# Kernel tuning notes

Hardware: AMD Instinct MI355X
Metric: run time of the kernel (lower is better)

Reference implementation:

```python
import jax, jax.numpy as jnp
import numpy as np

B, S, D, M, O = 16, 1024, 1024, 1024, 1024


def _sq_cdist(x1, x2):
    # squared euclidean distance, shapes (..., n, d) x (..., m, d) -> (..., n, m)
    n1 = jnp.sum(x1 * x1, axis=-1, keepdims=True)            # (..., n, 1)
    n2 = jnp.sum(x2 * x2, axis=-1)[..., None, :]             # (..., 1, m)
    cross = jnp.einsum('...nd,...md->...nm', x1, x2)
    return jnp.maximum(n1 + n2 - 2.0 * cross, 0.0)


def _rbf(x1, x2, log_lengthscale):
    ls2 = jnp.exp(log_lengthscale) ** 2
    return jnp.exp(-0.5 * _sq_cdist(x1, x2) / ls2)


def setup_inputs() -> dict:
    key = jax.random.key(0)
    k1, k2, k3 = jax.random.split(key, 3)
    x = jax.random.normal(k1, (B, S, D), dtype=jnp.float32)
    inducing_points = jax.random.normal(k2, (M, D), dtype=jnp.float32)
    log_lengthscale = jnp.zeros((1,), dtype=jnp.float32)
    log_noise = jnp.zeros((1,), dtype=jnp.float32)
    # nn.Linear(n_inducing, output_dim).weight has shape (O, M)
    lim = 1.0 / np.sqrt(M)
    W_out = jax.random.uniform(k3, (O, M), minval=-lim, maxval=lim, dtype=jnp.float32)
    return {
        'x': x,
        'inducing_points': inducing_points,
        'log_lengthscale': log_lengthscale,
        'log_noise': log_noise,
        'W_out': W_out,
        'num_sentences': S,
    }


def reference(x, inducing_points, log_lengthscale, log_noise, W_out, num_sentences):
    ll = log_lengthscale[0]
    K_xx = _rbf(x, x, ll)                                    # (B, S, S)
    K_xi = _rbf(x, inducing_points[None], ll)                # (B, S, M)
    K_ii = _rbf(inducing_points, inducing_points, ll)        # (M, M)
    K_ii_reg = K_ii + jnp.exp(log_noise[0]) * jnp.eye(M, dtype=x.dtype)
    K_ii_inv = jnp.linalg.inv(K_ii_reg)                      # (M, M)
    A = jnp.einsum('bsm,mk->bsk', K_xi, K_ii_inv)            # (B, S, M)
    mean = jnp.einsum('bsm,om->bso', A, W_out)               # (B, S, O)
    var = K_xx - jnp.einsum('bsm,btm->bst', A, K_xi)         # (B, S, S)
    var_diag = jnp.diagonal(var, axis1=-2, axis2=-1)         # (B, S)
    var_out = jnp.broadcast_to(var_diag[..., None], (x.shape[0], num_sentences, W_out.shape[0]))
    return mean, jax.nn.softplus(var_out)
```

## Files before the change

### kernel.cpp

```cpp
#include <hip/hip_runtime.h>
#include <hip/hip_bf16.h>
#include <math.h>


typedef unsigned short u16;
typedef __attribute__((ext_vector_type(8))) short short8;
typedef __attribute__((ext_vector_type(4))) float f32x4;
typedef __attribute__((ext_vector_type(4))) unsigned short us4;

__device__ __forceinline__ float bf2f(u16 b) {
  union { unsigned u; float f; } x; x.u = ((unsigned)b) << 16; return x.f;
}
__device__ __forceinline__ u16 f2bf(float f) {
  union { float f; unsigned u; } x; x.f = f;
  unsigned r = x.u + 0x7fffu + ((x.u >> 16) & 1u);
  return (u16)(r >> 16);
}

__device__ __forceinline__ void gl_lds16(const void* g, void* l) {
  __builtin_amdgcn_global_load_lds(
      (const __attribute__((address_space(1))) void*)g,
      (__attribute__((address_space(3))) void*)l, 16, 0, 0);
}

__device__ __forceinline__ float local_cmax(const float* rs, float* sm) {
  float m = 0.f;
  for (int i = threadIdx.x; i < 1024; i += 256) m = fmaxf(m, rs[i]);
#pragma unroll
  for (int o = 32; o > 0; o >>= 1) m = fmaxf(m, __shfl_xor(m, o));
  __syncthreads();
  if ((threadIdx.x & 63) == 0) sm[threadIdx.x >> 6] = m;
  __syncthreads();
  return 1.0f / fmaxf(fmaxf(sm[0], sm[1]), fmaxf(sm[2], sm[3]));
}

template <int EPI>
__device__ __forceinline__ void big_body(
    int bid, u16* lds,
    const u16* Ag, const u16* Bg,
    float* outF, float* varF, u16* outB,
    const float* rowN, const float* colN,
    const float* p_ll, float* qb) {
  constexpr int NT = 16;
  const int tid = threadIdx.x;
  const int lane = tid & 63;
  const int wave = tid >> 6;
  const int wr = wave >> 1, wc = wave & 1;
  const int fro = lane & 15, khi = lane >> 4;
  size_t brow, bcol;
  if (EPI == 3) {
    brow = (size_t)(bid >> 3);
    bcol = (size_t)(bid & 7);
  } else {
    const int xcd = bid & 7, j7 = bid >> 3;
    brow = (size_t)(xcd * 16 + (j7 >> 3));
    bcol = (size_t)(j7 & 7);
  }

  if (EPI == 0) {
    if (tid < 16) qb[(size_t)bid * 16 + tid] = 0.0f;
  }

  f32x4 acc[4][4] = {};

  auto stageA = [&](int tt, int bb) {
#pragma unroll
    for (int c = 0; c < 4; ++c) {
      const int ci = tid + 256 * c;
      const int row = ci >> 3;
      const int gk = (ci & 7) ^ (row & 7);
      gl_lds16(Ag + (size_t)(brow * 128 + row) * 1024 + tt * 64 + gk * 8,
               &lds[bb * 16384 + ci * 8]);
    }
  };
  auto stageB = [&](int tt, int bb) {
#pragma unroll
    for (int c = 0; c < 4; ++c) {
      const int ci = tid + 256 * c;
      const int row = ci >> 3;
      const int gk = (ci & 7) ^ (row & 7);
      gl_lds16(Bg + (size_t)(bcol * 128 + row) * 1024 + tt * 64 + gk * 8,
               &lds[bb * 16384 + 8192 + ci * 8]);
    }
  };

  stageA(0, 0);
  stageB(0, 0);
  stageB(1, 1);
  asm volatile("s_waitcnt vmcnt(4)" ::: "memory");
  __builtin_amdgcn_s_barrier();

  for (int t = 0; t < NT; ++t) {
    const int cb = t & 1;
    const int ab = cb * 16384;
    const int bb = cb * 16384 + 8192;
    short8 bfrag[4][2];
#pragma unroll
    for (int p = 0; p < 4; ++p) {
      short8 afr[2];
      const int rr = wr * 64 + p * 16 + fro;
#pragma unroll
      for (int s = 0; s < 2; ++s) {
        const int kl = (s * 4 + khi) ^ (rr & 7);
        afr[s] = *(const short8*)&lds[ab + (rr * 8 + kl) * 8];
      }
      if (p == 0) {
#pragma unroll
        for (int n = 0; n < 4; ++n) {
          const int cc = wc * 64 + n * 16 + fro;
#pragma unroll
          for (int s = 0; s < 2; ++s) {
            const int kl = (s * 4 + khi) ^ (cc & 7);
            bfrag[n][s] = *(const short8*)&lds[bb + (cc * 8 + kl) * 8];
          }
        }
        if (t + 1 < NT) stageA(t + 1, cb ^ 1);
      } else if (p == 1) {
        if (t + 2 < NT) stageB(t + 2, cb);
      }
      __builtin_amdgcn_s_setprio(1);
#pragma unroll
      for (int n = 0; n < 4; ++n)
#pragma unroll
        for (int s = 0; s < 2; ++s)
          acc[p][n] = __builtin_amdgcn_mfma_f32_16x16x32_bf16(
              afr[s], bfrag[n][s], acc[p][n], 0, 0, 0);
      __builtin_amdgcn_s_setprio(0);
      if (p == 3) {
        if (t < NT - 2) asm volatile("s_waitcnt vmcnt(4)" ::: "memory");
        else            asm volatile("s_waitcnt vmcnt(0)" ::: "memory");
      }
      __builtin_amdgcn_s_barrier();
    }
  }

  float inv2 = 0.f, cc2 = 0.f, ss2 = 0.f;
  if (EPI == 0) inv2 = 0.5f * expf(-2.0f * p_ll[0]);
  if (EPI == 3) {
    __syncthreads();
    cc2 = local_cmax(rowN, (float*)lds);
    ss2 = sqrtf(cc2);
  }
#pragma unroll
  for (int m = 0; m < 4; m++) {
#pragma unroll
    for (int j = 0; j < 4; j++) {
      const size_t grow = brow * 128 + wr * 64 + m * 16 + khi * 4 + j;
      float rn = 0.f, sp = 0.f;
      if (EPI == 0) rn = rowN[grow];
      if (EPI == 1) {
        float vq = 1.0f - qb[grow];
        sp = fmaxf(vq, 0.f) + log1pf(expf(-fabsf(vq)));
      }
      float part = 0.f;
#pragma unroll
      for (int n = 0; n < 4; n++) {
        const size_t gcol = bcol * 128 + wc * 64 + n * 16 + fro;
        const size_t o = grow * 1024 + gcol;
        float v = acc[m][n][j];
        if (EPI == 0) {
          float d2 = fmaxf(rn + colN[gcol] - 2.0f * v, 0.0f);
          outB[o] = f2bf(expf(-inv2 * d2));
        } else if (EPI == 1) {
          outF[o] = v;
          varF[o] = sp;
        } else if (EPI == 3) {
          float idv = (grow == gcol) ? 1.0f : 0.0f;
          outB[o] = f2bf(ss2 * (1.5f * idv - 0.5f * cc2 * bf2f(Ag[o]) +
                                0.6875f * bf2f(Bg[o]) - 0.3125f * cc2 * v));
        } else {
          part += v * v;
        }
      }
      if (EPI == 2) {
        part += __shfl_xor(part, 1);
        part += __shfl_xor(part, 2);
        part += __shfl_xor(part, 4);
        part += __shfl_xor(part, 8);
        if (fro == 0) atomicAdd(&qb[grow], part);
      }
    }
  }
}

__device__ __forceinline__ void small_core(const u16* Ap, const u16* Bp,
                                           u16* As, u16* Bs,
                                           f32x4 (&acc)[4][4]) {
  const int tid = threadIdx.x;
  const int lane = tid & 63;
  const int wave = tid >> 6;
  const int wr = wave >> 1, wc = wave & 1;
  const int idx0 = tid, idx1 = tid + 256;
  const u16* gA0 = Ap + (size_t)(idx0 >> 2) * 1024 + (size_t)(idx0 & 3) * 8;
  const u16* gA1 = Ap + (size_t)(idx1 >> 2) * 1024 + (size_t)(idx1 & 3) * 8;
  const u16* gB0 = Bp + (size_t)(idx0 >> 2) * 1024 + (size_t)(idx0 & 3) * 8;
  const u16* gB1 = Bp + (size_t)(idx1 >> 2) * 1024 + (size_t)(idx1 & 3) * 8;
  u16* lA0 = &As[idx0 * 8]; u16* lA1 = &As[idx1 * 8];
  u16* lB0 = &Bs[idx0 * 8]; u16* lB1 = &Bs[idx1 * 8];
  const int fro = lane & 15;
  const int ko = (lane >> 4) * 8;

  for (int kt = 0; kt < 1024; kt += 32) {
    gl_lds16(gA0 + kt, lA0);
    gl_lds16(gA1 + kt, lA1);
    gl_lds16(gB0 + kt, lB0);
    gl_lds16(gB1 + kt, lB1);
    __syncthreads();
    short8 af[4], bfr[4];
#pragma unroll
    for (int m = 0; m < 4; m++) {
      af[m]  = *(const short8*)&As[(wr * 64 + m * 16 + fro) * 32 + ko];
      bfr[m] = *(const short8*)&Bs[(wc * 64 + m * 16 + fro) * 32 + ko];
    }
#pragma unroll
    for (int m = 0; m < 4; m++)
#pragma unroll
      for (int n = 0; n < 4; n++)
        acc[m][n] = __builtin_amdgcn_mfma_f32_16x16x32_bf16(af[m], bfr[n], acc[m][n], 0, 0, 0);
    __syncthreads();
  }
}

__device__ __forceinline__ void kii_body(int bid, u16* lds,
                                         const u16* ipb, u16* kii,
                                         const float* ni, const float* ll,
                                         const float* ln, float* rs) {
  const int by = bid >> 3, bx = bid & 7;
  f32x4 acc[4][4] = {};
  small_core(ipb + (size_t)by * 131072, ipb + (size_t)bx * 131072,
             lds, lds + 4096, acc);
  const int lane = threadIdx.x & 63;
  const int wave = threadIdx.x >> 6;
  const int wr = wave >> 1, wc = wave & 1;
  float inv2 = 0.5f * expf(-2.0f * ll[0]);
  float noise = expf(ln[0]);
#pragma unroll
  for (int m = 0; m < 4; m++)
#pragma unroll
    for (int j = 0; j < 4; j++) {
      const size_t grow = by * 128 + wr * 64 + m * 16 + (lane >> 4) * 4 + j;
      float rn = ni[grow];
      float part = 0.f;
#pragma unroll
      for (int n = 0; n < 4; n++) {
        const size_t gcol = bx * 128 + wc * 64 + n * 16 + (lane & 15);
        float d2 = fmaxf(rn + ni[gcol] - 2.0f * acc[m][n][j], 0.0f);
        float kv = (grow == gcol) ? (1.0f + noise) : expf(-inv2 * d2);
        kii[grow * 1024 + gcol] = f2bf(kv);
        part += fabsf(kv);
      }
      part += __shfl_xor(part, 1);
      part += __shfl_xor(part, 2);
      part += __shfl_xor(part, 4);
      part += __shfl_xor(part, 8);
      if ((lane & 15) == 0) atomicAdd(&rs[grow], part);
    }
}

__device__ __forceinline__ void batch1_body(int bid, u16* lds,
                                            const u16* kii, const u16* Wb,
                                            u16* R2b, u16* T1b,
                                            const float* rs) {
  const int z = bid >> 6, r = bid & 63;
  const int by = r >> 3, bx = r & 7;
  f32x4 acc[4][4] = {};
  const u16* Abase = z ? Wb : kii;
  small_core(Abase + (size_t)by * 131072, kii + (size_t)bx * 131072,
             lds, lds + 4096, acc);
  __syncthreads();
  const float c = local_cmax(rs, (float*)lds);
  const int lane = threadIdx.x & 63;
  const int wave = threadIdx.x >> 6;
  const int wr = wave >> 1, wc = wave & 1;
#pragma unroll
  for (int m = 0; m < 4; m++)
#pragma unroll
    for (int j = 0; j < 4; j++) {
      const size_t grow = by * 128 + wr * 64 + m * 16 + (lane >> 4) * 4 + j;
#pragma unroll
      for (int n = 0; n < 4; n++) {
        const size_t gcol = bx * 128 + wc * 64 + n * 16 + (lane & 15);
        const size_t o = grow * 1024 + gcol;
        float v = acc[m][n][j];
        if (z == 0) {
          float idv = (grow == gcol) ? 1.0f : 0.0f;
          R2b[o] = f2bf(idv - 2.0f * c * bf2f(kii[o]) + c * c * v);
        } else {
          T1b[o] = f2bf(2.0f * bf2f(Wb[o]) - c * v);
        }
      }
    }
}

__device__ __forceinline__ void batch2b_body(int by, int bx, u16* lds,
                                             const u16* R2b, const u16* T1b,
                                             u16* U, const float* rs) {
  f32x4 acc[4][4] = {};
  small_core(T1b + (size_t)by * 131072, R2b + (size_t)bx * 131072,
             lds, lds + 4096, acc);
  __syncthreads();
  const float c = local_cmax(rs, (float*)lds);
  const int lane = threadIdx.x & 63;
  const int wave = threadIdx.x >> 6;
  const int wr = wave >> 1, wc = wave & 1;
#pragma unroll
  for (int m = 0; m < 4; m++)
#pragma unroll
    for (int j = 0; j < 4; j++) {
      const size_t grow = by * 128 + wr * 64 + m * 16 + (lane >> 4) * 4 + j;
#pragma unroll
      for (int n = 0; n < 4; n++) {
        const size_t gcol = bx * 128 + wc * 64 + n * 16 + (lane & 15);
        const size_t o = grow * 1024 + gcol;
        U[o + 1048576] = f2bf(c * (bf2f(T1b[o]) + acc[m][n][j]));
      }
    }
}

__device__ __forceinline__ void prepx_body(int bid, u16* lds,
                                           const float* x, u16* xbf,
                                           float* nx) {
  float* wsum = (float*)lds;
  for (int r = bid; r < 16384; r += 2048) {
    const float4 v = ((const float4*)(x + (size_t)r * 1024))[threadIdx.x];
    float ss = v.x * v.x + v.y * v.y + v.z * v.z + v.w * v.w;
    us4 o; o.x = f2bf(v.x); o.y = f2bf(v.y); o.z = f2bf(v.z); o.w = f2bf(v.w);
    ((us4*)(xbf + (size_t)r * 1024))[threadIdx.x] = o;
#pragma unroll
    for (int s = 32; s > 0; s >>= 1) ss += __shfl_xor(ss, s);
    if ((threadIdx.x & 63) == 0) wsum[threadIdx.x >> 6] = ss;
    __syncthreads();
    if (threadIdx.x == 0) nx[r] = wsum[0] + wsum[1] + wsum[2] + wsum[3];
    __syncthreads();
  }
}

__global__ __launch_bounds__(256) void fat1(
    const float* __restrict__ x, u16* __restrict__ xbf, float* __restrict__ nx,
    const u16* __restrict__ ipb, u16* __restrict__ kii,
    const float* __restrict__ ni, const float* __restrict__ ll,
    const float* __restrict__ ln, float* __restrict__ rs) {
  __shared__ u16 lds[8192];
  const int bid = blockIdx.x;
  if (bid < 64) kii_body(bid, lds, ipb, kii, ni, ll, ln, rs);
  else          prepx_body(bid - 64, lds, x, xbf, nx);
}

__global__ __launch_bounds__(256, 2) void fat2(
    const u16* __restrict__ xbf, const u16* __restrict__ ipb,
    u16* __restrict__ kxib,
    const float* __restrict__ nx, const float* __restrict__ ni,
    const float* __restrict__ ll, float* __restrict__ qb,
    const u16* __restrict__ kii, const u16* __restrict__ wbf,
    u16* __restrict__ R2b, u16* __restrict__ t1b,
    const float* __restrict__ rs) {
  __shared__ u16 lds[32768];
  const int bid = blockIdx.x;
  if (bid < 128) batch1_body(bid, lds, kii, wbf, R2b, t1b, rs);
  else big_body<0>(bid - 128, lds, xbf, ipb, nullptr, nullptr, kxib,
                   nx, ni, ll, qb);
}

__global__ __launch_bounds__(256, 2) void gemm_s(
    const u16* __restrict__ kii, const u16* __restrict__ R2b,
    u16* __restrict__ U, const float* __restrict__ rs) {
  __shared__ u16 lds[32768];
  big_body<3>(blockIdx.x, lds, kii, R2b, nullptr, nullptr, U,
              rs, nullptr, nullptr, nullptr);
}

__global__ __launch_bounds__(256, 2) void fat3(
    const u16* __restrict__ kxib, const u16* __restrict__ U,
    float* __restrict__ qb,
    const u16* __restrict__ R2b, const u16* __restrict__ t1b,
    u16* __restrict__ Uw, const float* __restrict__ rs) {
  __shared__ u16 lds[32768];
  const int bid = blockIdx.x;
  if (bid < 64) batch2b_body(bid >> 3, bid & 7, lds, R2b, t1b, Uw, rs);
  else big_body<2>(bid - 64, lds, kxib, U, nullptr, nullptr, nullptr,
                   nullptr, nullptr, nullptr, qb);
}

__global__ __launch_bounds__(256, 2) void kmean(
    const u16* __restrict__ kxib, const u16* __restrict__ w2t,
    float* __restrict__ meanO, float* __restrict__ varO,
    float* __restrict__ qb) {
  __shared__ u16 lds[32768];
  big_body<1>(blockIdx.x, lds, kxib, w2t, meanO, varO, nullptr,
              nullptr, nullptr, nullptr, qb);
}

__global__ __launch_bounds__(256) void prep_ipw(const float* __restrict__ ip,
                                                const float* __restrict__ W,
                                                u16* __restrict__ ipb,
                                                u16* __restrict__ wbf,
                                                float* __restrict__ ni,
                                                float* __restrict__ rs) {
  __shared__ float wsum[4];
  int b = blockIdx.x;
  if (b < 1024) {
    const float4 v = ((const float4*)(ip + (size_t)b * 1024))[threadIdx.x];
    float ss = v.x * v.x + v.y * v.y + v.z * v.z + v.w * v.w;
    us4 o; o.x = f2bf(v.x); o.y = f2bf(v.y); o.z = f2bf(v.z); o.w = f2bf(v.w);
    ((us4*)(ipb + (size_t)b * 1024))[threadIdx.x] = o;
#pragma unroll
    for (int s = 32; s > 0; s >>= 1) ss += __shfl_xor(ss, s);
    if ((threadIdx.x & 63) == 0) wsum[threadIdx.x >> 6] = ss;
    __syncthreads();
    if (threadIdx.x == 0) {
      ni[b] = wsum[0] + wsum[1] + wsum[2] + wsum[3];
      rs[b] = 0.0f;
    }
  } else {
    int r = b - 1024;
    const float4 v = ((const float4*)(W + (size_t)r * 1024))[threadIdx.x];
    us4 o; o.x = f2bf(v.x); o.y = f2bf(v.y); o.z = f2bf(v.z); o.w = f2bf(v.w);
    ((us4*)(wbf + (size_t)r * 1024))[threadIdx.x] = o;
  }
}

extern "C" void kernel_launch(void* const* d_in, const int* in_sizes, int n_in,
                              void* d_out, int out_size, void* d_ws, size_t ws_size,
                              hipStream_t stream) {
  const float* x  = (const float*)d_in[0];
  const float* ip = (const float*)d_in[1];
  const float* ll = (const float*)d_in[2];
  const float* ln = (const float*)d_in[3];
  const float* W  = (const float*)d_in[4];

  char* ws = (char*)d_ws;
  const size_t MB = 1ull << 20;
  u16* kxib = (u16*)(ws + 0 * MB);
  u16* xbf  = (u16*)(ws + 32 * MB);
  u16* ipb  = (u16*)(ws + 64 * MB);
  u16* wbf  = (u16*)(ws + 66 * MB);
  u16* kii  = (u16*)(ws + 68 * MB);
  u16* R2b  = (u16*)(ws + 70 * MB);
  u16* Ub   = (u16*)(ws + 74 * MB);
  u16* t1b  = (u16*)(ws + 78 * MB);
  float* nx = (float*)(ws + 80 * MB);
  float* qb = (float*)(ws + 80 * MB + 128 * 1024);
  float* ni = (float*)(ws + 80 * MB + 256 * 1024);
  float* rs = (float*)(ws + 80 * MB + 512 * 1024);

  float* meanO = (float*)d_out;
  float* varO  = meanO + 16777216ull;

  prep_ipw<<<2048, 256, 0, stream>>>(ip, W, ipb, wbf, ni, rs);

  fat1<<<2112, 256, 0, stream>>>(x, xbf, nx, ipb, kii, ni, ll, ln, rs);

  fat2<<<1152, 256, 0, stream>>>(xbf, ipb, kxib, nx, ni, ll, qb,
                                 kii, wbf, R2b, t1b, rs);

  gemm_s<<<64, 256, 0, stream>>>(kii, R2b, Ub, rs);

  fat3<<<1088, 256, 0, stream>>>(kxib, Ub, qb, R2b, t1b, Ub, rs);

  kmean<<<1024, 256, 0, stream>>>(kxib, Ub + 1048576, meanO, varO, qb);
}
```

Baseline: 203.1 us.

## Split variance writes into separate blocks and move W conversion into fat1

The softplus variance broadcast is moved out of the mean GEMM epilogue into 128 dedicated blocks that each write 128 rows with float4 stores, launched alongside the GEMM blocks in one kernel. The W-to-bf16 conversion moves from the first prep kernel into fat1 as extra blocks, so prep_ip only handles the inducing points. The goal is a lighter GEMM epilogue that stores only the mean, and less serialized work in the first launch. The cost is 128 blocks doing a purely store-bound pass that compete with GEMM blocks for CUs, plus a larger fat1 grid.

```diff
diff --git a/kernel.cpp b/kernel.cpp
--- a/kernel.cpp
+++ b/kernel.cpp
@@ -38,7 +38,7 @@
 __device__ __forceinline__ void big_body(
     int bid, u16* lds,
     const u16* Ag, const u16* Bg,
-    float* outF, float* varF, u16* outB,
+    float* outF, u16* outB,
     const float* rowN, const float* colN,
     const float* p_ll, float* qb) {
   constexpr int NT = 16;
@@ -146,12 +146,8 @@
 #pragma unroll
     for (int j = 0; j < 4; j++) {
       const size_t grow = brow * 128 + wr * 64 + m * 16 + khi * 4 + j;
-      float rn = 0.f, sp = 0.f;
+      float rn = 0.f;
       if (EPI == 0) rn = rowN[grow];
-      if (EPI == 1) {
-        float vq = 1.0f - qb[grow];
-        sp = fmaxf(vq, 0.f) + log1pf(expf(-fabsf(vq)));
-      }
       float part = 0.f;
 #pragma unroll
       for (int n = 0; n < 4; n++) {
@@ -163,7 +159,6 @@
           outB[o] = f2bf(expf(-inv2 * d2));
         } else if (EPI == 1) {
           outF[o] = v;
-          varF[o] = sp;
         } else if (EPI == 3) {
           float idv = (grow == gcol) ? 1.0f : 0.0f;
           outB[o] = f2bf(ss2 * (1.5f * idv - 0.5f * cc2 * bf2f(Ag[o]) +
@@ -335,15 +330,34 @@
   }
 }
 
+__device__ __forceinline__ void prepw_body(int r, const float* W, u16* wbf) {
+  const float4 v = ((const float4*)(W + (size_t)r * 1024))[threadIdx.x];
+  us4 o; o.x = f2bf(v.x); o.y = f2bf(v.y); o.z = f2bf(v.z); o.w = f2bf(v.w);
+  ((us4*)(wbf + (size_t)r * 1024))[threadIdx.x] = o;
+}
+
+__device__ __forceinline__ void var_body(int bid, const float* qb,
+                                         float* varO) {
+  for (int r = 0; r < 128; ++r) {
+    const int row = bid * 128 + r;
+    float vq = 1.0f - qb[row];
+    float sp = fmaxf(vq, 0.f) + log1pf(expf(-fabsf(vq)));
+    float4 o4 = {sp, sp, sp, sp};
+    ((float4*)(varO + (size_t)row * 1024))[threadIdx.x] = o4;
+  }
+}
+
 __global__ __launch_bounds__(256) void fat1(
     const float* __restrict__ x, u16* __restrict__ xbf, float* __restrict__ nx,
+    const float* __restrict__ W, u16* __restrict__ wbf,
     const u16* __restrict__ ipb, u16* __restrict__ kii,
     const float* __restrict__ ni, const float* __restrict__ ll,
     const float* __restrict__ ln, float* __restrict__ rs) {
   __shared__ u16 lds[8192];
   const int bid = blockIdx.x;
-  if (bid < 64) kii_body(bid, lds, ipb, kii, ni, ll, ln, rs);
-  else          prepx_body(bid - 64, lds, x, xbf, nx);
+  if (bid < 64)        kii_body(bid, lds, ipb, kii, ni, ll, ln, rs);
+  else if (bid < 2112) prepx_body(bid - 64, lds, x, xbf, nx);
+  else                 prepw_body(bid - 2112, W, wbf);
 }
 
 __global__ __launch_bounds__(256, 2) void fat2(
@@ -357,16 +371,15 @@
   __shared__ u16 lds[32768];
   const int bid = blockIdx.x;
   if (bid < 128) batch1_body(bid, lds, kii, wbf, R2b, t1b, rs);
-  else big_body<0>(bid - 128, lds, xbf, ipb, nullptr, nullptr, kxib,
-                   nx, ni, ll, qb);
+  else big_body<0>(bid - 128, lds, xbf, ipb, nullptr, kxib, nx, ni, ll, qb);
 }
 
 __global__ __launch_bounds__(256, 2) void gemm_s(
     const u16* __restrict__ kii, const u16* __restrict__ R2b,
     u16* __restrict__ U, const float* __restrict__ rs) {
   __shared__ u16 lds[32768];
-  big_body<3>(blockIdx.x, lds, kii, R2b, nullptr, nullptr, U,
-              rs, nullptr, nullptr, nullptr);
+  big_body<3>(blockIdx.x, lds, kii, R2b, nullptr, U, rs, nullptr, nullptr,
+              nullptr);
 }
 
 __global__ __launch_bounds__(256, 2) void fat3(
@@ -377,45 +390,38 @@
   __shared__ u16 lds[32768];
   const int bid = blockIdx.x;
   if (bid < 64) batch2b_body(bid >> 3, bid & 7, lds, R2b, t1b, Uw, rs);
-  else big_body<2>(bid - 64, lds, kxib, U, nullptr, nullptr, nullptr,
+  else big_body<2>(bid - 64, lds, kxib, U, nullptr, nullptr,
                    nullptr, nullptr, nullptr, qb);
 }
 
-__global__ __launch_bounds__(256, 2) void kmean(
+__global__ __launch_bounds__(256, 2) void fatmv(
     const u16* __restrict__ kxib, const u16* __restrict__ w2t,
     float* __restrict__ meanO, float* __restrict__ varO,
-    float* __restrict__ qb) {
+    const float* __restrict__ qb) {
   __shared__ u16 lds[32768];
-  big_body<1>(blockIdx.x, lds, kxib, w2t, meanO, varO, nullptr,
-              nullptr, nullptr, nullptr, qb);
-}
-
-__global__ __launch_bounds__(256) void prep_ipw(const float* __restrict__ ip,
-                                                const float* __restrict__ W,
-                                                u16* __restrict__ ipb,
-                                                u16* __restrict__ wbf,
-                                                float* __restrict__ ni,
-                                                float* __restrict__ rs) {
+  const int bid = blockIdx.x;
+  if (bid < 128) var_body(bid, qb, varO);
+  else big_body<1>(bid - 128, lds, kxib, w2t, meanO, nullptr,
+                   nullptr, nullptr, nullptr, nullptr);
+}
+
+__global__ __launch_bounds__(256) void prep_ip(const float* __restrict__ ip,
+                                               u16* __restrict__ ipb,
+                                               float* __restrict__ ni,
+                                               float* __restrict__ rs) {
   __shared__ float wsum[4];
   int b = blockIdx.x;
-  if (b < 1024) {
-    const float4 v = ((const float4*)(ip + (size_t)b * 1024))[threadIdx.x];
-    float ss = v.x * v.x + v.y * v.y + v.z * v.z + v.w * v.w;
-    us4 o; o.x = f2bf(v.x); o.y = f2bf(v.y); o.z = f2bf(v.z); o.w = f2bf(v.w);
-    ((us4*)(ipb + (size_t)b * 1024))[threadIdx.x] = o;
-#pragma unroll
-    for (int s = 32; s > 0; s >>= 1) ss += __shfl_xor(ss, s);
-    if ((threadIdx.x & 63) == 0) wsum[threadIdx.x >> 6] = ss;
-    __syncthreads();
-    if (threadIdx.x == 0) {
-      ni[b] = wsum[0] + wsum[1] + wsum[2] + wsum[3];
-      rs[b] = 0.0f;
-    }
-  } else {
-    int r = b - 1024;
-    const float4 v = ((const float4*)(W + (size_t)r * 1024))[threadIdx.x];
-    us4 o; o.x = f2bf(v.x); o.y = f2bf(v.y); o.z = f2bf(v.z); o.w = f2bf(v.w);
-    ((us4*)(wbf + (size_t)r * 1024))[threadIdx.x] = o;
+  const float4 v = ((const float4*)(ip + (size_t)b * 1024))[threadIdx.x];
+  float ss = v.x * v.x + v.y * v.y + v.z * v.z + v.w * v.w;
+  us4 o; o.x = f2bf(v.x); o.y = f2bf(v.y); o.z = f2bf(v.z); o.w = f2bf(v.w);
+  ((us4*)(ipb + (size_t)b * 1024))[threadIdx.x] = o;
+#pragma unroll
+  for (int s = 32; s > 0; s >>= 1) ss += __shfl_xor(ss, s);
+  if ((threadIdx.x & 63) == 0) wsum[threadIdx.x >> 6] = ss;
+  __syncthreads();
+  if (threadIdx.x == 0) {
+    ni[b] = wsum[0] + wsum[1] + wsum[2] + wsum[3];
+    rs[b] = 0.0f;
   }
 }
 
@@ -446,9 +452,9 @@
   float* meanO = (float*)d_out;
   float* varO  = meanO + 16777216ull;
 
-  prep_ipw<<<2048, 256, 0, stream>>>(ip, W, ipb, wbf, ni, rs);
-
-  fat1<<<2112, 256, 0, stream>>>(x, xbf, nx, ipb, kii, ni, ll, ln, rs);
+  prep_ip<<<1024, 256, 0, stream>>>(ip, ipb, ni, rs);
+
+  fat1<<<3136, 256, 0, stream>>>(x, xbf, nx, W, wbf, ipb, kii, ni, ll, ln, rs);
 
   fat2<<<1152, 256, 0, stream>>>(xbf, ipb, kxib, nx, ni, ll, qb,
                                  kii, wbf, R2b, t1b, rs);
@@ -457,5 +463,5 @@
 
   fat3<<<1088, 256, 0, stream>>>(kxib, Ub, qb, R2b, t1b, Ub, rs);
 
-  kmean<<<1024, 256, 0, stream>>>(kxib, Ub + 1048576, meanO, varO, qb);
-}
+  fatmv<<<1152, 256, 0, stream>>>(kxib, Ub + 1048576, meanO, varO, qb);
+}
```

After: 208.3 us. 1.03x slower.
